# Kernel optimization log

Measured on AMD Instinct MI355X. Metric: run time of the kernel, lower is better.

Reference implementation:

```python
import jax, jax.numpy as jnp
import numpy as np

GAMMA = 2.0
SPATIAL_WEIGHT = 0.01
NUM_CLASSES = 10
NUM_TISSUES = 5
N_NODES = 50000
K_CLUSTERS = 32
N_EDGES = 1600000
BATCH = 4096


def setup_inputs() -> dict:
    key = jax.random.key(0)
    ks = jax.random.split(key, 8)
    logits = jax.random.normal(ks[0], (BATCH, NUM_CLASSES), dtype=jnp.float32)
    targets = jax.random.randint(ks[1], (BATCH,), 0, NUM_CLASSES)
    S = jax.random.normal(ks[2], (N_NODES, K_CLUSTERS), dtype=jnp.float32)
    positions = jax.random.normal(ks[3], (N_NODES, 2), dtype=jnp.float32)
    edge_index = jax.random.randint(ks[4], (2, N_EDGES), 0, N_NODES)
    tissue_types = jax.random.randint(ks[5], (BATCH,), 0, NUM_TISSUES)
    # learned-ish fixed weighting buffers (registered buffers in torch)
    class_weights = jnp.asarray([1.0, 0.8, 1.2, 1.5, 0.9, 1.1, 1.0, 0.7, 1.3, 1.0], dtype=jnp.float32)
    tissue_weights = jnp.asarray([1.0, 1.2, 0.9, 1.1, 0.8], dtype=jnp.float32)
    return {
        "logits": logits,
        "targets": targets,
        "S": S,
        "positions": positions,
        "edge_index": edge_index,
        "tissue_types": tissue_types,
        "class_weights": class_weights,
        "tissue_weights": tissue_weights,
    }


def reference(logits, targets, S, positions, edge_index, tissue_types, class_weights, tissue_weights):
    # ---- Focal loss (Eq. 1): -sum w_c * w_t * (1-p)^gamma * log p ----
    log_probs = jax.nn.log_softmax(logits, axis=-1)              # [B, C]
    lp_t = jnp.take_along_axis(log_probs, targets[:, None], axis=1)[:, 0]  # [B]
    p_t = jnp.exp(lp_t)
    focal_w = (1.0 - p_t) ** GAMMA
    focal_w = focal_w * class_weights[targets] * tissue_weights[tissue_types]
    cls_loss = jnp.mean(-focal_w * lp_t)

    # ---- Spatial regularization: vectorized over edges & clusters ----
    src, dst = edge_index[0], edge_index[1]                      # [E]
    diff = positions[src] - positions[dst]                       # [E, 2]
    d2 = jnp.sum(diff * diff, axis=-1)                           # [E]  (||.||)^2
    Si = S[src]                                                  # [E, K]
    Sj = S[dst]                                                  # [E, K]
    pair = jnp.where((Si > 0) & (Sj > 0), Si * Sj, 0.0)          # mask S[i,k]>0 and S[j,k]>0
    spatial = SPATIAL_WEIGHT * jnp.sum(jnp.sum(pair, axis=-1) * d2) / edge_index.shape[1]

    total = cls_loss + spatial
    return total, cls_loss, spatial
```

## Files before the change

### kernel.cpp

```cpp
#include <hip/hip_runtime.h>
#include <math.h>

#define NUM_CLASSES 10

typedef __attribute__((ext_vector_type(2))) float f32x2;

__device__ __forceinline__ double block_reduce_sum(double v, double* lds) {
    #pragma unroll
    for (int off = 32; off > 0; off >>= 1)
        v += __shfl_down(v, off, 64);
    int lane = threadIdx.x & 63;
    int wid  = threadIdx.x >> 6;
    int nw   = blockDim.x >> 6;
    if (lane == 0) lds[wid] = v;
    __syncthreads();
    if (wid == 0) {
        v = (lane < nw) ? lds[lane] : 0.0;
        #pragma unroll
        for (int off = 4; off > 0; off >>= 1)
            v += __shfl_down(v, off, 64);
    }
    return v;
}

__device__ __forceinline__ double focal_term(
    const float* __restrict__ logits, const int* __restrict__ targets,
    const int* __restrict__ tissue, const float* __restrict__ cw,
    const float* __restrict__ tw, int r) {
    const float* row = logits + (size_t)r * NUM_CLASSES;
    float l[NUM_CLASSES];
    float m = -INFINITY;
    #pragma unroll
    for (int c = 0; c < NUM_CLASSES; ++c) { l[c] = row[c]; m = fmaxf(m, l[c]); }
    float s = 0.f;
    #pragma unroll
    for (int c = 0; c < NUM_CLASSES; ++c) s += expf(l[c] - m);
    int   t  = targets[r];
    float lp = l[t] - m - logf(s);
    float p  = expf(lp);
    float om = 1.f - p;
    float w  = om * om * cw[t] * tw[tissue[r]];
    return (double)(-w * lp);
}

__device__ __forceinline__ float fp8dot4(int a, int b, float d) {
    f32x2 al = __builtin_amdgcn_cvt_pk_f32_fp8(a, false);
    f32x2 ah = __builtin_amdgcn_cvt_pk_f32_fp8(a, true);
    f32x2 bl = __builtin_amdgcn_cvt_pk_f32_fp8(b, false);
    f32x2 bh = __builtin_amdgcn_cvt_pk_f32_fp8(b, true);
    d = fmaf(al.x, bl.x, d); d = fmaf(al.y, bl.y, d);
    d = fmaf(ah.x, bh.x, d); d = fmaf(ah.y, bh.y, d);
    return d;
}

__device__ __forceinline__ float fp8dot32(int4 a0, int4 a1, int4 b0, int4 b1) {
    float dot = 0.f;
    dot = fp8dot4(a0.x, b0.x, dot);
    dot = fp8dot4(a0.y, b0.y, dot);
    dot = fp8dot4(a0.z, b0.z, dot);
    dot = fp8dot4(a0.w, b0.w, dot);
    dot = fp8dot4(a1.x, b1.x, dot);
    dot = fp8dot4(a1.y, b1.y, dot);
    dot = fp8dot4(a1.z, b1.z, dot);
    dot = fp8dot4(a1.w, b1.w, dot);
    return dot;
}

__global__ void pack_kernel(const float4* __restrict__ S4,
                            const float2* __restrict__ pos,
                            int* __restrict__ rec_i,
                            int n4, int N) {
    int i = blockIdx.x * blockDim.x + threadIdx.x;
    if (i < n4) {
        float4 v = S4[i];
        int w = __builtin_amdgcn_cvt_pk_fp8_f32(fmaxf(v.x, 0.f), fmaxf(v.y, 0.f), 0, false);
        w = __builtin_amdgcn_cvt_pk_fp8_f32(fmaxf(v.z, 0.f), fmaxf(v.w, 0.f), w, true);
        int node = i >> 3, sub = i & 7;
        rec_i[node * 16 + sub] = w;
    }
    if (i < N) {
        float2 p = pos[i];
        rec_i[i * 16 + 8] = __float_as_int(p.x);
        rec_i[i * 16 + 9] = __float_as_int(p.y);
    }
}

__global__ __launch_bounds__(256) void spatial_focal_kernel(
    const float* __restrict__ logits,
    const int*   __restrict__ targets,
    const int*   __restrict__ tissue,
    const float* __restrict__ cw,
    const float* __restrict__ tw,
    const int4*  __restrict__ rec,
    const int*   __restrict__ src_idx,
    const int*   __restrict__ dst_idx,
    int B, int E, int T,
    double*      __restrict__ part_f,
    double*      __restrict__ part_s) {

    __shared__ double lds_f[4];
    __shared__ double lds_s[4];
    int gtid = blockIdx.x * blockDim.x + threadIdx.x;

    double fl = 0.0;
    if (gtid < B) fl = focal_term(logits, targets, tissue, cw, tw, gtid);

    int e0 = gtid, e1 = gtid + T, e2 = gtid + 2 * T, e3 = gtid + 3 * T;
    float m0 = (e0 < E) ? 1.f : 0.f;
    float m1 = (e1 < E) ? 1.f : 0.f;
    float m2 = (e2 < E) ? 1.f : 0.f;
    float m3 = (e3 < E) ? 1.f : 0.f;
    int e0c = (e0 < E) ? e0 : 0;
    int e1c = (e1 < E) ? e1 : 0;
    int e2c = (e2 < E) ? e2 : 0;
    int e3c = (e3 < E) ? e3 : 0;

    int s0 = src_idx[e0c], d0 = dst_idx[e0c];
    int s1 = src_idx[e1c], d1 = dst_idx[e1c];
    int s2 = src_idx[e2c], d2 = dst_idx[e2c];
    int s3 = src_idx[e3c], d3 = dst_idx[e3c];

    const int4 *q;
    q = rec + (size_t)s0 * 4; int4 as0 = q[0], as0h = q[1]; float2 ps0 = *(const float2*)(q + 2);
    q = rec + (size_t)d0 * 4; int4 bs0 = q[0], bs0h = q[1]; float2 pd0 = *(const float2*)(q + 2);
    q = rec + (size_t)s1 * 4; int4 as1 = q[0], as1h = q[1]; float2 ps1 = *(const float2*)(q + 2);
    q = rec + (size_t)d1 * 4; int4 bs1 = q[0], bs1h = q[1]; float2 pd1 = *(const float2*)(q + 2);
    q = rec + (size_t)s2 * 4; int4 as2 = q[0], as2h = q[1]; float2 ps2 = *(const float2*)(q + 2);
    q = rec + (size_t)d2 * 4; int4 bs2 = q[0], bs2h = q[1]; float2 pd2 = *(const float2*)(q + 2);
    q = rec + (size_t)s3 * 4; int4 as3 = q[0], as3h = q[1]; float2 ps3 = *(const float2*)(q + 2);
    q = rec + (size_t)d3 * 4; int4 bs3 = q[0], bs3h = q[1]; float2 pd3 = *(const float2*)(q + 2);

    double sp = 0.0;
    float dx, dy, w;
    w = fp8dot32(as0, as0h, bs0, bs0h);
    dx = ps0.x - pd0.x; dy = ps0.y - pd0.y;
    sp += (double)(m0 * w * (dx * dx + dy * dy));
    w = fp8dot32(as1, as1h, bs1, bs1h);
    dx = ps1.x - pd1.x; dy = ps1.y - pd1.y;
    sp += (double)(m1 * w * (dx * dx + dy * dy));
    w = fp8dot32(as2, as2h, bs2, bs2h);
    dx = ps2.x - pd2.x; dy = ps2.y - pd2.y;
    sp += (double)(m2 * w * (dx * dx + dy * dy));
    w = fp8dot32(as3, as3h, bs3, bs3h);
    dx = ps3.x - pd3.x; dy = ps3.y - pd3.y;
    sp += (double)(m3 * w * (dx * dx + dy * dy));

    double bs_f = block_reduce_sum(fl, lds_f);
    double bs_s = block_reduce_sum(sp, lds_s);
    if (threadIdx.x == 0) {
        part_f[blockIdx.x] = bs_f;
        part_s[blockIdx.x] = bs_s;
    }
}

__global__ void reduce_kernel(const double* __restrict__ part_f,
                              const double* __restrict__ part_s,
                              int nb, float* __restrict__ out, int B, int E) {
    __shared__ double lds_f[4];
    __shared__ double lds_s[4];
    double f = 0.0, s = 0.0;
    for (int i = threadIdx.x; i < nb; i += blockDim.x) {
        f += part_f[i];
        s += part_s[i];
    }
    double tf = block_reduce_sum(f, lds_f);
    double ts = block_reduce_sum(s, lds_s);
    if (threadIdx.x == 0) {
        float cls = (float)(tf / (double)B);
        float spv = (float)(0.01 * ts / (double)E);
        out[0] = cls + spv;
        out[1] = cls;
        out[2] = spv;
    }
}

__global__ __launch_bounds__(256) void fallback_kernel(
    const float*  __restrict__ logits,
    const int*    __restrict__ targets,
    const int*    __restrict__ tissue,
    const float*  __restrict__ cw,
    const float*  __restrict__ tw,
    const float4* __restrict__ S4,
    const float2* __restrict__ pos,
    const int*    __restrict__ src_idx,
    const int*    __restrict__ dst_idx,
    int B, int E, int T,
    double*       __restrict__ part_f,
    double*       __restrict__ part_s) {
    __shared__ double lds_f[4];
    __shared__ double lds_s[4];
    int gtid = blockIdx.x * blockDim.x + threadIdx.x;
    double fl = 0.0;
    if (gtid < B) fl = focal_term(logits, targets, tissue, cw, tw, gtid);
    double sp = 0.0;
    for (int e = gtid; e < E; e += T) {
        int s = src_idx[e], d = dst_idx[e];
        const float4* Sr = S4 + (size_t)s * 8;
        const float4* Dr = S4 + (size_t)d * 8;
        float dot = 0.f;
        #pragma unroll
        for (int c = 0; c < 8; ++c) {
            float4 a = Sr[c], b = Dr[c];
            dot += fmaxf(a.x, 0.f) * fmaxf(b.x, 0.f);
            dot += fmaxf(a.y, 0.f) * fmaxf(b.y, 0.f);
            dot += fmaxf(a.z, 0.f) * fmaxf(b.z, 0.f);
            dot += fmaxf(a.w, 0.f) * fmaxf(b.w, 0.f);
        }
        float2 pp = pos[s], qq = pos[d];
        float dx = pp.x - qq.x, dy = pp.y - qq.y;
        sp += (double)(dot * (dx * dx + dy * dy));
    }
    double bs_f = block_reduce_sum(fl, lds_f);
    double bs_s = block_reduce_sum(sp, lds_s);
    if (threadIdx.x == 0) {
        part_f[blockIdx.x] = bs_f;
        part_s[blockIdx.x] = bs_s;
    }
}

extern "C" void kernel_launch(void* const* d_in, const int* in_sizes, int n_in,
                              void* d_out, int out_size, void* d_ws, size_t ws_size,
                              hipStream_t stream) {
    const float* logits  = (const float*)d_in[0];
    const int*   targets = (const int*)  d_in[1];
    const float* S       = (const float*)d_in[2];
    const float* pos     = (const float*)d_in[3];
    const int*   edge    = (const int*)  d_in[4];
    const int*   tissue  = (const int*)  d_in[5];
    const float* cw      = (const float*)d_in[6];
    const float* tw      = (const float*)d_in[7];
    float* out = (float*)d_out;

    int B  = in_sizes[1];
    int E  = in_sizes[4] / 2;
    int nS = in_sizes[2];
    int N  = in_sizes[3] / 2;
    int n4 = nS / 4;

    const int EDGES_PER_THREAD = 4;
    int nb = (E + 256 * EDGES_PER_THREAD - 1) / (256 * EDGES_PER_THREAD);
    int T  = nb * 256;

    size_t rec_bytes = (size_t)N * 64;
    size_t part_off  = (rec_bytes + 255) & ~(size_t)255;
    size_t need      = part_off + (size_t)2 * nb * sizeof(double) + 256;

    if (ws_size >= need) {
        int*    rec    = (int*)d_ws;
        double* part_f = (double*)((char*)d_ws + part_off);
        double* part_s = part_f + nb;
        int packN = (n4 > N) ? n4 : N;
        pack_kernel<<<(packN + 255) / 256, 256, 0, stream>>>(
            (const float4*)S, (const float2*)pos, rec, n4, N);
        spatial_focal_kernel<<<nb, 256, 0, stream>>>(
            logits, targets, tissue, cw, tw,
            (const int4*)rec, edge, edge + E,
            B, E, T, part_f, part_s);
        reduce_kernel<<<1, 256, 0, stream>>>(part_f, part_s, nb, out, B, E);
    } else {
        int nb2 = 2048;
        int T2  = nb2 * 256;
        double* part_f = (double*)d_ws;
        double* part_s = part_f + nb2;
        fallback_kernel<<<nb2, 256, 0, stream>>>(
            logits, targets, tissue, cw, tw,
            (const float4*)S, (const float2*)pos, edge, edge + E,
            B, E, T2, part_f, part_s);
        reduce_kernel<<<1, 256, 0, stream>>>(part_f, part_s, nb2, out, B, E);
    }
}
```

Measured before the change: 108.5 us.

## Split each edge across a thread pair sharing gathers via lane shuffles

Each edge is now handled by two adjacent lanes. One lane loads the src index and the other the dst index, and they swap them with shuffles. Each lane gathers only half of the 32-byte fp8 cluster record for both endpoints plus one position, and the partial dot products and positions are combined through xor shuffles. This doubles the thread count (twice the blocks) and halves the per-thread gather footprint to raise memory-level parallelism and occupancy. The cost is extra shuffles and edges being counted twice before the final 0.5 scale.

```diff
diff --git a/kernel.cpp b/kernel.cpp
--- a/kernel.cpp
+++ b/kernel.cpp
@@ -53,16 +53,12 @@
     return d;
 }
 
-__device__ __forceinline__ float fp8dot32(int4 a0, int4 a1, int4 b0, int4 b1) {
+__device__ __forceinline__ float fp8dot16(int4 a, int4 b) {
     float dot = 0.f;
-    dot = fp8dot4(a0.x, b0.x, dot);
-    dot = fp8dot4(a0.y, b0.y, dot);
-    dot = fp8dot4(a0.z, b0.z, dot);
-    dot = fp8dot4(a0.w, b0.w, dot);
-    dot = fp8dot4(a1.x, b1.x, dot);
-    dot = fp8dot4(a1.y, b1.y, dot);
-    dot = fp8dot4(a1.z, b1.z, dot);
-    dot = fp8dot4(a1.w, b1.w, dot);
+    dot = fp8dot4(a.x, b.x, dot);
+    dot = fp8dot4(a.y, b.y, dot);
+    dot = fp8dot4(a.z, b.z, dot);
+    dot = fp8dot4(a.w, b.w, dot);
     return dot;
 }
 
@@ -85,6 +81,8 @@
     }
 }
 
+#define EPT 4
+
 __global__ __launch_bounds__(256) void spatial_focal_kernel(
     const float* __restrict__ logits,
     const int*   __restrict__ targets,
@@ -94,7 +92,7 @@
     const int4*  __restrict__ rec,
     const int*   __restrict__ src_idx,
     const int*   __restrict__ dst_idx,
-    int B, int E, int T,
+    int B, int E, int G,
     double*      __restrict__ part_f,
     double*      __restrict__ part_s) {
 
@@ -105,45 +103,54 @@
     double fl = 0.0;
     if (gtid < B) fl = focal_term(logits, targets, tissue, cw, tw, gtid);
 
-    int e0 = gtid, e1 = gtid + T, e2 = gtid + 2 * T, e3 = gtid + 3 * T;
-    float m0 = (e0 < E) ? 1.f : 0.f;
-    float m1 = (e1 < E) ? 1.f : 0.f;
-    float m2 = (e2 < E) ? 1.f : 0.f;
-    float m3 = (e3 < E) ? 1.f : 0.f;
-    int e0c = (e0 < E) ? e0 : 0;
-    int e1c = (e1 < E) ? e1 : 0;
-    int e2c = (e2 < E) ? e2 : 0;
-    int e3c = (e3 < E) ? e3 : 0;
-
-    int s0 = src_idx[e0c], d0 = dst_idx[e0c];
-    int s1 = src_idx[e1c], d1 = dst_idx[e1c];
-    int s2 = src_idx[e2c], d2 = dst_idx[e2c];
-    int s3 = src_idx[e3c], d3 = dst_idx[e3c];
-
-    const int4 *q;
-    q = rec + (size_t)s0 * 4; int4 as0 = q[0], as0h = q[1]; float2 ps0 = *(const float2*)(q + 2);
-    q = rec + (size_t)d0 * 4; int4 bs0 = q[0], bs0h = q[1]; float2 pd0 = *(const float2*)(q + 2);
-    q = rec + (size_t)s1 * 4; int4 as1 = q[0], as1h = q[1]; float2 ps1 = *(const float2*)(q + 2);
-    q = rec + (size_t)d1 * 4; int4 bs1 = q[0], bs1h = q[1]; float2 pd1 = *(const float2*)(q + 2);
-    q = rec + (size_t)s2 * 4; int4 as2 = q[0], as2h = q[1]; float2 ps2 = *(const float2*)(q + 2);
-    q = rec + (size_t)d2 * 4; int4 bs2 = q[0], bs2h = q[1]; float2 pd2 = *(const float2*)(q + 2);
-    q = rec + (size_t)s3 * 4; int4 as3 = q[0], as3h = q[1]; float2 ps3 = *(const float2*)(q + 2);
-    q = rec + (size_t)d3 * 4; int4 bs3 = q[0], bs3h = q[1]; float2 pd3 = *(const float2*)(q + 2);
+    int p = gtid & 1;
+    int g = gtid >> 1;
+    const int* mybase = p ? dst_idx : src_idx;
+
+    int   ec[EPT];
+    float msk[EPT];
+    #pragma unroll
+    for (int j = 0; j < EPT; ++j) {
+        int e  = g + j * G;
+        msk[j] = (e < E) ? 1.f : 0.f;
+        ec[j]  = (e < E) ? e : 0;
+    }
+
+    int mine[EPT];
+    #pragma unroll
+    for (int j = 0; j < EPT; ++j) mine[j] = mybase[ec[j]];
+
+    int s_[EPT], d_[EPT];
+    #pragma unroll
+    for (int j = 0; j < EPT; ++j) {
+        int other = __shfl_xor(mine[j], 1, 64);
+        s_[j] = p ? other  : mine[j];
+        d_[j] = p ? mine[j] : other;
+    }
+
+    int4   rs[EPT], rd[EPT];
+    float2 pm[EPT];
+    #pragma unroll
+    for (int j = 0; j < EPT; ++j) {
+        const int4* qs = rec + (size_t)s_[j] * 4;
+        const int4* qd = rec + (size_t)d_[j] * 4;
+        rs[j] = qs[p];
+        rd[j] = qd[p];
+        pm[j] = *(const float2*)((p ? qd : qs) + 2);
+    }
 
     double sp = 0.0;
-    float dx, dy, w;
-    w = fp8dot32(as0, as0h, bs0, bs0h);
-    dx = ps0.x - pd0.x; dy = ps0.y - pd0.y;
-    sp += (double)(m0 * w * (dx * dx + dy * dy));
-    w = fp8dot32(as1, as1h, bs1, bs1h);
-    dx = ps1.x - pd1.x; dy = ps1.y - pd1.y;
-    sp += (double)(m1 * w * (dx * dx + dy * dy));
-    w = fp8dot32(as2, as2h, bs2, bs2h);
-    dx = ps2.x - pd2.x; dy = ps2.y - pd2.y;
-    sp += (double)(m2 * w * (dx * dx + dy * dy));
-    w = fp8dot32(as3, as3h, bs3, bs3h);
-    dx = ps3.x - pd3.x; dy = ps3.y - pd3.y;
-    sp += (double)(m3 * w * (dx * dx + dy * dy));
+    #pragma unroll
+    for (int j = 0; j < EPT; ++j) {
+        float dh  = fp8dot16(rs[j], rd[j]);
+        float dot = dh + __shfl_xor(dh, 1, 64);
+        float ox  = __shfl_xor(pm[j].x, 1, 64);
+        float oy  = __shfl_xor(pm[j].y, 1, 64);
+        float dx  = pm[j].x - ox;
+        float dy  = pm[j].y - oy;
+        sp += (double)(msk[j] * dot * (dx * dx + dy * dy));
+    }
+    sp *= 0.5;
 
     double bs_f = block_reduce_sum(fl, lds_f);
     double bs_s = block_reduce_sum(sp, lds_s);
@@ -237,9 +244,8 @@
     int N  = in_sizes[3] / 2;
     int n4 = nS / 4;
 
-    const int EDGES_PER_THREAD = 4;
-    int nb = (E + 256 * EDGES_PER_THREAD - 1) / (256 * EDGES_PER_THREAD);
-    int T  = nb * 256;
+    int nb = (E + 128 * EPT - 1) / (128 * EPT);
+    int G  = nb * 128;
 
     size_t rec_bytes = (size_t)N * 64;
     size_t part_off  = (rec_bytes + 255) & ~(size_t)255;
@@ -255,7 +261,7 @@
         spatial_focal_kernel<<<nb, 256, 0, stream>>>(
             logits, targets, tissue, cw, tw,
             (const int4*)rec, edge, edge + E,
-            B, E, T, part_f, part_s);
+            B, E, G, part_f, part_s);
         reduce_kernel<<<1, 256, 0, stream>>>(part_f, part_s, nb, out, B, E);
     } else {
         int nb2 = 2048;
```

Result: slower. 115.9 us (+6.8%).

## Quantize cluster assignments to per-node 4-bit nibbles with integer dot products

Applied to the files above, without the earlier changes.

Replaces the fp8 packing of the ReLU'd S rows with per-node scaled 4-bit quantization: 32 clusters fit in 16 bytes, with position and scale stored alongside in a 32-byte record. The edge kernel computes the masked pair sum with udot4 integer dot products over nibble lanes and rescales by the product of the two node scales. This halves the bytes gathered per edge endpoint and replaces the fp8-to-float conversions with integer dot instructions. The cost is much coarser precision, with only 16 levels per node, which risks exceeding the accuracy tolerance. The pack kernel now runs one thread per node with strided row reads.

```diff
diff --git a/kernel.cpp b/kernel.cpp
--- a/kernel.cpp
+++ b/kernel.cpp
@@ -2,8 +2,6 @@
 #include <math.h>
 
 #define NUM_CLASSES 10
-
-typedef __attribute__((ext_vector_type(2))) float f32x2;
 
 __device__ __forceinline__ double block_reduce_sum(double v, double* lds) {
     #pragma unroll
@@ -43,46 +41,66 @@
     return (double)(-w * lp);
 }
 
-__device__ __forceinline__ float fp8dot4(int a, int b, float d) {
-    f32x2 al = __builtin_amdgcn_cvt_pk_f32_fp8(a, false);
-    f32x2 ah = __builtin_amdgcn_cvt_pk_f32_fp8(a, true);
-    f32x2 bl = __builtin_amdgcn_cvt_pk_f32_fp8(b, false);
-    f32x2 bh = __builtin_amdgcn_cvt_pk_f32_fp8(b, true);
-    d = fmaf(al.x, bl.x, d); d = fmaf(al.y, bl.y, d);
-    d = fmaf(ah.x, bh.x, d); d = fmaf(ah.y, bh.y, d);
-    return d;
-}
-
-__device__ __forceinline__ float fp8dot32(int4 a0, int4 a1, int4 b0, int4 b1) {
-    float dot = 0.f;
-    dot = fp8dot4(a0.x, b0.x, dot);
-    dot = fp8dot4(a0.y, b0.y, dot);
-    dot = fp8dot4(a0.z, b0.z, dot);
-    dot = fp8dot4(a0.w, b0.w, dot);
-    dot = fp8dot4(a1.x, b1.x, dot);
-    dot = fp8dot4(a1.y, b1.y, dot);
-    dot = fp8dot4(a1.z, b1.z, dot);
-    dot = fp8dot4(a1.w, b1.w, dot);
-    return dot;
+__device__ __forceinline__ unsigned udot4(unsigned a, unsigned b, unsigned c) {
+#if __has_builtin(__builtin_amdgcn_udot4)
+    return __builtin_amdgcn_udot4(a, b, c, false);
+#else
+    c += (a & 0xFFu) * (b & 0xFFu);
+    c += ((a >> 8)  & 0xFFu) * ((b >> 8)  & 0xFFu);
+    c += ((a >> 16) & 0xFFu) * ((b >> 16) & 0xFFu);
+    c += (a >> 24) * (b >> 24);
+    return c;
+#endif
+}
+
+__device__ __forceinline__ unsigned nibdot(int4 ra, int4 rb) {
+    unsigned acc = 0;
+    const unsigned M = 0x0F0F0F0Fu;
+    #pragma unroll
+    for (int k = 0; k < 4; ++k) {
+        unsigned a = (k == 0) ? (unsigned)ra.x : (k == 1) ? (unsigned)ra.y
+                   : (k == 2) ? (unsigned)ra.z : (unsigned)ra.w;
+        unsigned b = (k == 0) ? (unsigned)rb.x : (k == 1) ? (unsigned)rb.y
+                   : (k == 2) ? (unsigned)rb.z : (unsigned)rb.w;
+        acc = udot4(a & M, b & M, acc);
+        acc = udot4((a >> 4) & M, (b >> 4) & M, acc);
+    }
+    return acc;
 }
 
 __global__ void pack_kernel(const float4* __restrict__ S4,
                             const float2* __restrict__ pos,
                             int* __restrict__ rec_i,
-                            int n4, int N) {
-    int i = blockIdx.x * blockDim.x + threadIdx.x;
-    if (i < n4) {
-        float4 v = S4[i];
-        int w = __builtin_amdgcn_cvt_pk_fp8_f32(fmaxf(v.x, 0.f), fmaxf(v.y, 0.f), 0, false);
-        w = __builtin_amdgcn_cvt_pk_fp8_f32(fmaxf(v.z, 0.f), fmaxf(v.w, 0.f), w, true);
-        int node = i >> 3, sub = i & 7;
-        rec_i[node * 16 + sub] = w;
-    }
-    if (i < N) {
-        float2 p = pos[i];
-        rec_i[i * 16 + 8] = __float_as_int(p.x);
-        rec_i[i * 16 + 9] = __float_as_int(p.y);
-    }
+                            int N) {
+    int node = blockIdx.x * blockDim.x + threadIdx.x;
+    if (node >= N) return;
+    const float4* row = S4 + (size_t)node * 8;
+    float v[32];
+    float m = 0.f;
+    #pragma unroll
+    for (int c = 0; c < 8; ++c) {
+        float4 q = row[c];
+        v[4*c+0] = fmaxf(q.x, 0.f); v[4*c+1] = fmaxf(q.y, 0.f);
+        v[4*c+2] = fmaxf(q.z, 0.f); v[4*c+3] = fmaxf(q.w, 0.f);
+        m = fmaxf(m, v[4*c+0]); m = fmaxf(m, v[4*c+1]);
+        m = fmaxf(m, v[4*c+2]); m = fmaxf(m, v[4*c+3]);
+    }
+    float scale = m * (1.f / 15.f);
+    float inv   = (m > 0.f) ? (15.f / m) : 0.f;
+    unsigned w[4] = {0u, 0u, 0u, 0u};
+    #pragma unroll
+    for (int i = 0; i < 32; ++i) {
+        unsigned n = (unsigned)(int)rintf(v[i] * inv);
+        n = n > 15u ? 15u : n;
+        w[i >> 3] |= n << (4 * (i & 7));
+    }
+    int* r = rec_i + (size_t)node * 8;
+    float2 p = pos[node];
+    r[0] = (int)w[0]; r[1] = (int)w[1]; r[2] = (int)w[2]; r[3] = (int)w[3];
+    r[4] = __float_as_int(p.x);
+    r[5] = __float_as_int(p.y);
+    r[6] = __float_as_int(scale);
+    r[7] = 0;
 }
 
 __global__ __launch_bounds__(256) void spatial_focal_kernel(
@@ -121,28 +139,28 @@
     int s3 = src_idx[e3c], d3 = dst_idx[e3c];
 
     const int4 *q;
-    q = rec + (size_t)s0 * 4; int4 as0 = q[0], as0h = q[1]; float2 ps0 = *(const float2*)(q + 2);
-    q = rec + (size_t)d0 * 4; int4 bs0 = q[0], bs0h = q[1]; float2 pd0 = *(const float2*)(q + 2);
-    q = rec + (size_t)s1 * 4; int4 as1 = q[0], as1h = q[1]; float2 ps1 = *(const float2*)(q + 2);
-    q = rec + (size_t)d1 * 4; int4 bs1 = q[0], bs1h = q[1]; float2 pd1 = *(const float2*)(q + 2);
-    q = rec + (size_t)s2 * 4; int4 as2 = q[0], as2h = q[1]; float2 ps2 = *(const float2*)(q + 2);
-    q = rec + (size_t)d2 * 4; int4 bs2 = q[0], bs2h = q[1]; float2 pd2 = *(const float2*)(q + 2);
-    q = rec + (size_t)s3 * 4; int4 as3 = q[0], as3h = q[1]; float2 ps3 = *(const float2*)(q + 2);
-    q = rec + (size_t)d3 * 4; int4 bs3 = q[0], bs3h = q[1]; float2 pd3 = *(const float2*)(q + 2);
+    q = rec + (size_t)s0 * 2; int4 ra0 = q[0]; float4 xa0 = *(const float4*)(q + 1);
+    q = rec + (size_t)d0 * 2; int4 rb0 = q[0]; float4 xb0 = *(const float4*)(q + 1);
+    q = rec + (size_t)s1 * 2; int4 ra1 = q[0]; float4 xa1 = *(const float4*)(q + 1);
+    q = rec + (size_t)d1 * 2; int4 rb1 = q[0]; float4 xb1 = *(const float4*)(q + 1);
+    q = rec + (size_t)s2 * 2; int4 ra2 = q[0]; float4 xa2 = *(const float4*)(q + 1);
+    q = rec + (size_t)d2 * 2; int4 rb2 = q[0]; float4 xb2 = *(const float4*)(q + 1);
+    q = rec + (size_t)s3 * 2; int4 ra3 = q[0]; float4 xa3 = *(const float4*)(q + 1);
+    q = rec + (size_t)d3 * 2; int4 rb3 = q[0]; float4 xb3 = *(const float4*)(q + 1);
 
     double sp = 0.0;
     float dx, dy, w;
-    w = fp8dot32(as0, as0h, bs0, bs0h);
-    dx = ps0.x - pd0.x; dy = ps0.y - pd0.y;
+    w = (float)nibdot(ra0, rb0) * (xa0.z * xb0.z);
+    dx = xa0.x - xb0.x; dy = xa0.y - xb0.y;
     sp += (double)(m0 * w * (dx * dx + dy * dy));
-    w = fp8dot32(as1, as1h, bs1, bs1h);
-    dx = ps1.x - pd1.x; dy = ps1.y - pd1.y;
+    w = (float)nibdot(ra1, rb1) * (xa1.z * xb1.z);
+    dx = xa1.x - xb1.x; dy = xa1.y - xb1.y;
     sp += (double)(m1 * w * (dx * dx + dy * dy));
-    w = fp8dot32(as2, as2h, bs2, bs2h);
-    dx = ps2.x - pd2.x; dy = ps2.y - pd2.y;
+    w = (float)nibdot(ra2, rb2) * (xa2.z * xb2.z);
+    dx = xa2.x - xb2.x; dy = xa2.y - xb2.y;
     sp += (double)(m2 * w * (dx * dx + dy * dy));
-    w = fp8dot32(as3, as3h, bs3, bs3h);
-    dx = ps3.x - pd3.x; dy = ps3.y - pd3.y;
+    w = (float)nibdot(ra3, rb3) * (xa3.z * xb3.z);
+    dx = xa3.x - xb3.x; dy = xa3.y - xb3.y;
     sp += (double)(m3 * w * (dx * dx + dy * dy));
 
     double bs_f = block_reduce_sum(fl, lds_f);
@@ -231,17 +249,15 @@
     const float* tw      = (const float*)d_in[7];
     float* out = (float*)d_out;
 
-    int B  = in_sizes[1];
-    int E  = in_sizes[4] / 2;
-    int nS = in_sizes[2];
-    int N  = in_sizes[3] / 2;
-    int n4 = nS / 4;
+    int B = in_sizes[1];
+    int E = in_sizes[4] / 2;
+    int N = in_sizes[3] / 2;
 
     const int EDGES_PER_THREAD = 4;
     int nb = (E + 256 * EDGES_PER_THREAD - 1) / (256 * EDGES_PER_THREAD);
     int T  = nb * 256;
 
-    size_t rec_bytes = (size_t)N * 64;
+    size_t rec_bytes = (size_t)N * 32;
     size_t part_off  = (rec_bytes + 255) & ~(size_t)255;
     size_t need      = part_off + (size_t)2 * nb * sizeof(double) + 256;
 
@@ -249,9 +265,8 @@
         int*    rec    = (int*)d_ws;
         double* part_f = (double*)((char*)d_ws + part_off);
         double* part_s = part_f + nb;
-        int packN = (n4 > N) ? n4 : N;
-        pack_kernel<<<(packN + 255) / 256, 256, 0, stream>>>(
-            (const float4*)S, (const float2*)pos, rec, n4, N);
+        pack_kernel<<<(N + 255) / 256, 256, 0, stream>>>(
+            (const float4*)S, (const float2*)pos, rec, N);
         spatial_focal_kernel<<<nb, 256, 0, stream>>>(
             logits, targets, tissue, cw, tw,
             (const int4*)rec, edge, edge + E,
```

New measurement: 103.6 us. -4.6%, faster.
